# Performance work log

Hardware: AMD Instinct MI355X
Metric: run time of the kernel (lower is better)

## Reference

```python
import jax, jax.numpy as jnp
import numpy as np

EMBED_DIM = 1024
NUM_HEADS = 16
HEAD_DIM = EMBED_DIM // NUM_HEADS


def setup_inputs() -> dict:
    key = jax.random.key(0)
    ks = jax.random.split(key, 9)
    B, S, E, Hd = 1, 4096, EMBED_DIM, HEAD_DIM
    s = 0.02
    return {
        "x": jax.random.normal(ks[0], (B, S, E), jnp.float32),
        "mask": jnp.ones((B, S, S), jnp.int32),
        "Wq": jax.random.normal(ks[1], (E, E), jnp.float32) * s,
        "bq": jnp.zeros((E,), jnp.float32),
        "Wk": jax.random.normal(ks[2], (E, Hd), jnp.float32) * s,
        "bk": jnp.zeros((Hd,), jnp.float32),
        "Wv": jax.random.normal(ks[3], (E, Hd), jnp.float32) * s,
        "bv": jnp.zeros((Hd,), jnp.float32),
        "Wo": jax.random.normal(ks[4], (E, E), jnp.float32) * s,
        "bo": jnp.zeros((E,), jnp.float32),
    }


def reference(x, mask, Wq, bq, Wk, bk, Wv, bv, Wo, bo):
    B, S, E = x.shape
    H, Hd = NUM_HEADS, HEAD_DIM
    q = (x @ Wq + bq).reshape(B, S, H, Hd).transpose(0, 2, 1, 3)  # [B,H,S,Hd]
    k = x @ Wk + bk  # [B,S,Hd] single KV head (MQA)
    v = x @ Wv + bv  # [B,S,Hd]
    scale = 1.0 / np.sqrt(Hd).astype(np.float32)
    # broadcast single-head K across all query heads
    qk = jnp.einsum('bhqd,bkd->bhqk', q, k) * scale  # [B,H,S,S]
    qk = jnp.where(mask[:, None, :, :] == 0, jnp.float32(-10000.0), qk)
    attn = jax.nn.softmax(qk, axis=-1)
    out = jnp.einsum('bhqk,bkd->bhqd', attn, v)  # [B,H,S,Hd]
    out = out.transpose(0, 2, 1, 3).reshape(B, S, E)
    return out @ Wo + bo
```

## Files before the change

### kernel.cpp

```cpp
#include <hip/hip_runtime.h>
#include <hip/hip_bf16.h>
#include <stdint.h>

typedef __bf16 bf16x8 __attribute__((ext_vector_type(8)));
typedef float f32x4 __attribute__((ext_vector_type(4)));
typedef float f32x16 __attribute__((ext_vector_type(16)));
typedef unsigned int uint2v __attribute__((ext_vector_type(2)));

#define E_DIM 1024
#define HD 64
#define NH 16
#define QKV_LD 1152
#define LOG2E 1.44269504088896f

__device__ __forceinline__ float toF(float x) { return x; }
__device__ __forceinline__ float toF(__hip_bfloat16 x) { return __bfloat162float(x); }
__device__ __forceinline__ void storeOut(float* p, float v) { *p = v; }
__device__ __forceinline__ void storeOut(__hip_bfloat16* p, float v) { *p = __float2bfloat16(v); }

__device__ __forceinline__ unsigned cvtpk_bf16(float lo, float hi_) {
    unsigned r;
    asm("v_cvt_pk_bf16_f32 %0, %1, %2" : "=v"(r) : "v"(lo), "v"(hi_));
    return r;
}
__device__ __forceinline__ void perm32swap(unsigned& a, unsigned& b) {
    uint2v r = __builtin_amdgcn_permlane32_swap(a, b, false, false);
    a = r.x; b = r.y;
}
__device__ __forceinline__ float fexp2(float x) {
    float r;
    asm("v_exp_f32 %0, %1" : "=v"(r) : "v"(x));
    return r;
}

typedef __attribute__((address_space(1))) void gvoid;
typedef __attribute__((address_space(3))) void lvoid;
__device__ __forceinline__ void gload_lds16(const void* g, void* l) {
    __builtin_amdgcn_global_load_lds((gvoid*)g, (lvoid*)l, 16, 0, 0);
}

__global__ void cast_f32_bf16_kernel(const float* __restrict__ in, __hip_bfloat16* __restrict__ o, int n) {
    int i = (blockIdx.x * blockDim.x + threadIdx.x) * 4;
    if (i + 3 < n) {
        float4 v = *reinterpret_cast<const float4*>(in + i);
        __hip_bfloat16 t[4] = {__float2bfloat16(v.x), __float2bfloat16(v.y),
                               __float2bfloat16(v.z), __float2bfloat16(v.w)};
        *reinterpret_cast<uint2*>(o + i) = *reinterpret_cast<uint2*>(t);
    }
}

template<typename InT>
__global__ void transpose_cast_kernel(const InT* __restrict__ in, int ldi,
                                      __hip_bfloat16* __restrict__ out, int ldo,
                                      int R, int C) {
    __shared__ float tile[32][33];
    const int bx = blockIdx.x * 32;
    const int by = blockIdx.y * 32;
    const int tx = threadIdx.x & 31, ty = threadIdx.x >> 5;
#pragma unroll
    for (int j = 0; j < 4; ++j) {
        int r = bx + ty + j * 8, c = by + tx;
        tile[ty + j * 8][tx] = toF(in[(size_t)r * ldi + c]);
    }
    __syncthreads();
#pragma unroll
    for (int j = 0; j < 4; ++j) {
        int c = by + ty + j * 8, r = bx + tx;
        out[(size_t)c * ldo + r] = __float2bfloat16(tile[tx][ty + j * 8]);
    }
}

__global__ void concat_bias3_kernel(const float* __restrict__ bq, const float* __restrict__ bk,
                                    const float* __restrict__ bv, float* __restrict__ bqkv) {
    int i = blockIdx.x * blockDim.x + threadIdx.x;
    if (i < E_DIM) bqkv[i] = bq[i];
    else if (i < E_DIM + HD) bqkv[i] = bk[i - E_DIM];
    else if (i < E_DIM + 2 * HD) bqkv[i] = bv[i - E_DIM - HD];
}

__global__ void maskbits_kernel(const int* __restrict__ mask, unsigned long long* __restrict__ mb,
                                int nwords) {
    int gtid = blockIdx.x * blockDim.x + threadIdx.x;
    int wid = gtid >> 6, lane = gtid & 63;
    int nw = (gridDim.x * blockDim.x) >> 6;
    for (int w = wid; w < nwords; w += nw) {
        int v = mask[(size_t)w * 64 + lane];
        unsigned long long b = __ballot(v != 0);
        if (lane == 0) mb[w] = b;
    }
}

template<typename OutT>
__global__ __launch_bounds__(256)
void gemm_bt2_kernel(const __hip_bfloat16* __restrict__ A,
                     const __hip_bfloat16* __restrict__ Bt,
                     const float* __restrict__ bias,
                     OutT* __restrict__ C,
                     int M, int N, int K, float sQ, int nQ, float sKV) {
    constexpr int BM = 128, BN = 128, BK = 64;
    __shared__ __align__(16) unsigned char lA[2][BM * BK * 2];
    __shared__ __align__(16) unsigned char lB[2][BN * BK * 2];
    const int ntn = N / BN;
    const int tm = blockIdx.x / ntn, tn = blockIdx.x % ntn;
    const int tid = threadIdx.x, lane = tid & 63, wave = tid >> 6;
    const int l15 = lane & 15, l4 = lane >> 4;
    const int wm = (wave >> 1) * 64, wn = (wave & 1) * 64;
    const int r0 = tm * BM, c0 = tn * BN;
    const int NK = K / BK;

    size_t aoff[4], boff[4];
    unsigned ldso[4];
#pragma unroll
    for (int i = 0; i < 4; ++i) {
        int row = wave * 32 + i * 8 + (lane >> 3);
        int c = (lane & 7) ^ (row & 7);
        aoff[i] = (size_t)(r0 + row) * K * 2 + c * 16;
        boff[i] = (size_t)(c0 + row) * K * 2 + c * 16;
        ldso[i] = wave * 4096 + i * 1024;
    }
    const char* Ab = (const char*)A;
    const char* Bb = (const char*)Bt;

#pragma unroll
    for (int i = 0; i < 4; ++i) {
        gload_lds16(Ab + aoff[i], &lA[0][ldso[i]]);
        gload_lds16(Bb + boff[i], &lB[0][ldso[i]]);
    }
    __syncthreads();

    f32x4 z4 = {0.f, 0.f, 0.f, 0.f};
    f32x4 acc[4][4];
#pragma unroll
    for (int mi = 0; mi < 4; ++mi)
#pragma unroll
        for (int ni = 0; ni < 4; ++ni) acc[mi][ni] = z4;

    int buf = 0;
    for (int ks = 0; ks < NK; ++ks) {
        if (ks + 1 < NK) {
            size_t kb = (size_t)(ks + 1) * BK * 2;
#pragma unroll
            for (int i = 0; i < 4; ++i) {
                gload_lds16(Ab + aoff[i] + kb, &lA[buf ^ 1][ldso[i]]);
                gload_lds16(Bb + boff[i] + kb, &lB[buf ^ 1][ldso[i]]);
            }
        }
        bf16x8 af[4][2], bf[4][2];
#pragma unroll
        for (int mi = 0; mi < 4; ++mi) {
            int row = wm + mi * 16 + l15;
#pragma unroll
            for (int kh = 0; kh < 2; ++kh) {
                int slot = (kh * 4 + l4) ^ (row & 7);
                af[mi][kh] = *reinterpret_cast<const bf16x8*>(&lA[buf][row * 128 + slot * 16]);
            }
        }
#pragma unroll
        for (int ni = 0; ni < 4; ++ni) {
            int row = wn + ni * 16 + l15;
#pragma unroll
            for (int kh = 0; kh < 2; ++kh) {
                int slot = (kh * 4 + l4) ^ (row & 7);
                bf[ni][kh] = *reinterpret_cast<const bf16x8*>(&lB[buf][row * 128 + slot * 16]);
            }
        }
        __builtin_amdgcn_s_setprio(1);
#pragma unroll
        for (int mi = 0; mi < 4; ++mi)
#pragma unroll
            for (int ni = 0; ni < 4; ++ni) {
                acc[mi][ni] = __builtin_amdgcn_mfma_f32_16x16x32_bf16(af[mi][0], bf[ni][0], acc[mi][ni], 0, 0, 0);
                acc[mi][ni] = __builtin_amdgcn_mfma_f32_16x16x32_bf16(af[mi][1], bf[ni][1], acc[mi][ni], 0, 0, 0);
            }
        __builtin_amdgcn_s_setprio(0);
        __syncthreads();
        buf ^= 1;
    }

#pragma unroll
    for (int ni = 0; ni < 4; ++ni) {
        int col = c0 + wn + ni * 16 + l15;
        float b = bias[col];
        float s = (col < nQ) ? sQ : sKV;
#pragma unroll
        for (int mi = 0; mi < 4; ++mi) {
            int row = r0 + wm + mi * 16 + l4 * 4;
#pragma unroll
            for (int r = 0; r < 4; ++r) {
                float v = (acc[mi][ni][r] + b) * s;
                storeOut(C + (size_t)(row + r) * N + col, v);
            }
        }
    }
}

__global__ __launch_bounds__(256, 2)
void mqa5_kernel(const __hip_bfloat16* __restrict__ qkv,
                 const __hip_bfloat16* __restrict__ vtb,
                 const unsigned long long* __restrict__ mbits,
                 __hip_bfloat16* __restrict__ attnb,
                 int S) {
    __shared__ __align__(16) unsigned char sKV[2][32768];
    const int tid = threadIdx.x, lane = tid & 63, w = tid >> 6;
    const int r31 = lane & 31, hi = lane >> 5, rx = r31 & 15;
    const int q0 = blockIdx.x * 32;
    const int h = blockIdx.y * 4 + w;
    const int NT = S / 128, NW64 = S / 64;
    const __hip_bfloat16* kvb = qkv + E_DIM;

    bf16x8 qf[4];
    {
        const __hip_bfloat16* qp = qkv + (size_t)(q0 + r31) * QKV_LD + h * HD + hi * 8;
#pragma unroll
        for (int s = 0; s < 4; ++s) qf[s] = *reinterpret_cast<const bf16x8*>(qp + 16 * s);
    }

    const char* gbase[8];
    int gstep[8];
    unsigned ldsoff[8];
#pragma unroll
    for (int i = 0; i < 8; ++i) {
        int r = w * 32 + i * 4 + (lane >> 4);
        int sl = lane & 15;
        int c = sl ^ (r & 15);
        if (c < 8) {
            gbase[i] = (const char*)(kvb + (size_t)r * QKV_LD + c * 8);
            gstep[i] = 128 * QKV_LD * 2;
        } else {
            gbase[i] = (const char*)(vtb + (size_t)(r & 63) * S + (r >> 6) * 64 + (c - 8) * 8);
            gstep[i] = 128 * 2;
        }
        ldsoff[i] = w * 8192 + i * 1024;
    }

#pragma unroll
    for (int i = 0; i < 8; ++i) { gload_lds16(gbase[i], &sKV[0][ldsoff[i]]); gbase[i] += gstep[i]; }
    __syncthreads();

    float rm = -3e38f, rl = 0.f;
    f32x16 oacc[2];
#pragma unroll
    for (int i = 0; i < 16; ++i) { oacc[0][i] = 0.f; oacc[1][i] = 0.f; }

    int buf = 0;
    for (int t = 0; t < NT; ++t) {
        if (t + 1 < NT) {
#pragma unroll
            for (int i = 0; i < 8; ++i) { gload_lds16(gbase[i], &sKV[buf ^ 1][ldsoff[i]]); gbase[i] += gstep[i]; }
        }
        ulonglong2 wb = *reinterpret_cast<const ulonglong2*>(
            mbits + (size_t)(q0 + r31) * NW64 + 2 * t);
        const unsigned char* bp = sKV[buf];

        f32x16 sacc[4];
        __builtin_amdgcn_s_setprio(1);
#pragma unroll
        for (int kb = 0; kb < 4; ++kb) {
            const unsigned char* rowp = bp + (kb * 32 + r31) * 256;
            f32x16 a;
#pragma unroll
            for (int i = 0; i < 16; ++i) a[i] = 0.f;
#pragma unroll
            for (int s = 0; s < 4; ++s) {
                int slot = (2 * s + hi) ^ rx;
                bf16x8 kf = *reinterpret_cast<const bf16x8*>(rowp + slot * 16);
                a = __builtin_amdgcn_mfma_f32_32x32x16_bf16(kf, qf[s], a, 0, 0, 0);
            }
            sacc[kb] = a;
        }
        __builtin_amdgcn_s_setprio(0);

        if ((wb.x & wb.y) != ~0ull) {
#pragma unroll
            for (int kb = 0; kb < 4; ++kb) {
                unsigned long long wv = (kb < 2) ? wb.x : wb.y;
                int base = (kb & 1) * 32;
#pragma unroll
                for (int r = 0; r < 16; ++r) {
                    int kl = base + (r & 3) + 8 * (r >> 2) + 4 * hi;
                    if (!((wv >> kl) & 1)) sacc[kb][r] = -14427.0f;
                }
            }
        }

        float t0[8];
#pragma unroll
        for (int j = 0; j < 8; ++j) {
            float a01 = fmaxf(fmaxf(sacc[0][j], sacc[0][j + 8]), fmaxf(sacc[1][j], sacc[1][j + 8]));
            float a23 = fmaxf(fmaxf(sacc[2][j], sacc[2][j + 8]), fmaxf(sacc[3][j], sacc[3][j + 8]));
            t0[j] = fmaxf(a01, a23);
        }
        float u0 = fmaxf(t0[0], t0[4]), u1 = fmaxf(t0[1], t0[5]);
        float u2 = fmaxf(t0[2], t0[6]), u3 = fmaxf(t0[3], t0[7]);
        float pmax = fmaxf(fmaxf(u0, u1), fmaxf(u2, u3));
        pmax = fmaxf(pmax, __shfl_xor(pmax, 32));

        if (!__all(pmax - rm <= 8.0f)) {
            float rmn = fmaxf(rm, pmax);
            float al = fexp2(rm - rmn);
            rl *= al;
#pragma unroll
            for (int r = 0; r < 16; ++r) { oacc[0][r] *= al; oacc[1][r] *= al; }
            rm = rmn;
        }

        float s0 = 0.f, s1 = 0.f, s2 = 0.f, s3 = 0.f;
#pragma unroll
        for (int kb = 0; kb < 4; ++kb) {
#pragma unroll
            for (int r = 0; r < 16; r += 4) {
                sacc[kb][r + 0] = fexp2(sacc[kb][r + 0] - rm); s0 += sacc[kb][r + 0];
                sacc[kb][r + 1] = fexp2(sacc[kb][r + 1] - rm); s1 += sacc[kb][r + 1];
                sacc[kb][r + 2] = fexp2(sacc[kb][r + 2] - rm); s2 += sacc[kb][r + 2];
                sacc[kb][r + 3] = fexp2(sacc[kb][r + 3] - rm); s3 += sacc[kb][r + 3];
            }
        }
        float sum = (s0 + s1) + (s2 + s3);
        sum += __shfl_xor(sum, 32);
        rl += sum;

        bf16x8 pa[8];
#pragma unroll
        for (int kb = 0; kb < 4; ++kb) {
#pragma unroll
            for (int half = 0; half < 2; ++half) {
                int b0 = half * 8;
                unsigned A = cvtpk_bf16(sacc[kb][b0 + 0], sacc[kb][b0 + 1]);
                unsigned B = cvtpk_bf16(sacc[kb][b0 + 2], sacc[kb][b0 + 3]);
                unsigned C = cvtpk_bf16(sacc[kb][b0 + 4], sacc[kb][b0 + 5]);
                unsigned D = cvtpk_bf16(sacc[kb][b0 + 6], sacc[kb][b0 + 7]);
                perm32swap(A, C);
                perm32swap(B, D);
                union { unsigned u[4]; bf16x8 v; } pk;
                pk.u[0] = A; pk.u[1] = B; pk.u[2] = C; pk.u[3] = D;
                pa[kb * 2 + half] = pk.v;
            }
        }

        __builtin_amdgcn_s_setprio(1);
#pragma unroll
        for (int db = 0; db < 2; ++db) {
            f32x16 a = oacc[db];
#pragma unroll
            for (int j = 0; j < 2; ++j) {
                const unsigned char* rowp = bp + (j * 64 + db * 32 + r31) * 256;
#pragma unroll
                for (int s = 0; s < 4; ++s) {
                    int slot = (8 + 2 * s + hi) ^ rx;
                    bf16x8 vf = *reinterpret_cast<const bf16x8*>(rowp + slot * 16);
                    a = __builtin_amdgcn_mfma_f32_32x32x16_bf16(vf, pa[j * 4 + s], a, 0, 0, 0);
                }
            }
            oacc[db] = a;
        }
        __builtin_amdgcn_s_setprio(0);

        __syncthreads();
        buf ^= 1;
    }

    float inv = 1.0f / rl;
    __hip_bfloat16* op = attnb + (size_t)(q0 + r31) * E_DIM + h * HD;
#pragma unroll
    for (int db = 0; db < 2; ++db)
#pragma unroll
        for (int m = 0; m < 4; ++m) {
            uint2 pk;
            pk.x = cvtpk_bf16(oacc[db][4 * m + 0] * inv, oacc[db][4 * m + 1] * inv);
            pk.y = cvtpk_bf16(oacc[db][4 * m + 2] * inv, oacc[db][4 * m + 3] * inv);
            *reinterpret_cast<uint2*>(op + db * 32 + m * 8 + hi * 4) = pk;
        }
}

extern "C" void kernel_launch(void* const* d_in, const int* in_sizes, int n_in,
                              void* d_out, int out_size, void* d_ws, size_t ws_size,
                              hipStream_t stream) {
    (void)n_in; (void)out_size; (void)ws_size;
    const float* x  = (const float*)d_in[0];
    const int* mask = (const int*)d_in[1];
    const float* Wq = (const float*)d_in[2];
    const float* bq = (const float*)d_in[3];
    const float* Wk = (const float*)d_in[4];
    const float* bk = (const float*)d_in[5];
    const float* Wv = (const float*)d_in[6];
    const float* bv = (const float*)d_in[7];
    const float* Wo = (const float*)d_in[8];
    const float* bo = (const float*)d_in[9];
    float* out = (float*)d_out;

    const int E = E_DIM;
    const int S = in_sizes[0] / E;

    char* ws = (char*)d_ws;
    size_t off = 0;
    auto alloc = [&](size_t b) { char* p = ws + off; off += (b + 255) & ~(size_t)255; return p; };
    __hip_bfloat16* xb     = (__hip_bfloat16*)alloc((size_t)S * E * 2);
    __hip_bfloat16* wqkvT  = (__hip_bfloat16*)alloc((size_t)QKV_LD * E * 2);
    __hip_bfloat16* woT    = (__hip_bfloat16*)alloc((size_t)E * E * 2);
    __hip_bfloat16* qkvb   = (__hip_bfloat16*)alloc((size_t)S * QKV_LD * 2);
    __hip_bfloat16* vtb    = (__hip_bfloat16*)alloc((size_t)HD * S * 2);
    __hip_bfloat16* attnb  = (__hip_bfloat16*)alloc((size_t)S * E * 2);
    float* bqkv  = (float*)alloc(QKV_LD * 4);
    unsigned long long* mbits = (unsigned long long*)alloc((size_t)S * (S / 64) * 8);

    cast_f32_bf16_kernel<<<dim3((S * E / 4 + 255) / 256), dim3(256), 0, stream>>>(x, xb, S * E);
    transpose_cast_kernel<float><<<dim3(E / 32, E / 32), dim3(256), 0, stream>>>(Wq, E, wqkvT, E, E, E);
    transpose_cast_kernel<float><<<dim3(E / 32, HD / 32), dim3(256), 0, stream>>>(
        Wk, HD, wqkvT + (size_t)E * E, E, E, HD);
    transpose_cast_kernel<float><<<dim3(E / 32, HD / 32), dim3(256), 0, stream>>>(
        Wv, HD, wqkvT + (size_t)(E + HD) * E, E, E, HD);
    transpose_cast_kernel<float><<<dim3(E / 32, E / 32), dim3(256), 0, stream>>>(Wo, E, woT, E, E, E);
    concat_bias3_kernel<<<dim3((QKV_LD + 255) / 256), dim3(256), 0, stream>>>(bq, bk, bv, bqkv);
    maskbits_kernel<<<dim3(1024), dim3(256), 0, stream>>>(mask, mbits, S * (S / 64));

    gemm_bt2_kernel<__hip_bfloat16><<<dim3((S / 128) * (QKV_LD / 128)), dim3(256), 0, stream>>>(
        xb, wqkvT, bqkv, qkvb, S, QKV_LD, E, 0.125f * LOG2E, E, 1.0f);
    transpose_cast_kernel<__hip_bfloat16><<<dim3(S / 32, HD / 32), dim3(256), 0, stream>>>(
        qkvb + E + HD, QKV_LD, vtb, S, S, HD);
    mqa5_kernel<<<dim3(S / 32, NH / 4), dim3(256), 0, stream>>>(qkvb, vtb, mbits, attnb, S);
    gemm_bt2_kernel<float><<<dim3((S / 128) * (E / 128)), dim3(256), 0, stream>>>(
        attnb, woT, bo, out, S, E, E, 1.0f, E, 1.0f);
}
```

Baseline: 181.1 us.

## Compute softmax row sums with MFMA, merge weight transposes, restructure PV loop

```diff
diff --git a/kernel.cpp b/kernel.cpp
--- a/kernel.cpp
+++ b/kernel.cpp
@@ -67,6 +67,35 @@
     for (int j = 0; j < 4; ++j) {
         int c = by + ty + j * 8, r = bx + tx;
         out[(size_t)c * ldo + r] = __float2bfloat16(tile[tx][ty + j * 8]);
+    }
+}
+
+__global__ __launch_bounds__(256)
+void transpose4_kernel(const float* __restrict__ Wq, const float* __restrict__ Wk,
+                       const float* __restrict__ Wv, const float* __restrict__ Wo,
+                       __hip_bfloat16* __restrict__ wqkvT, __hip_bfloat16* __restrict__ woT) {
+    const int z = blockIdx.z;
+    const float* in; __hip_bfloat16* out; int ldi;
+    if (z == 0)      { in = Wq; out = wqkvT;                                ldi = E_DIM; }
+    else if (z == 1) { if (blockIdx.y >= HD / 32) return;
+                       in = Wk; out = wqkvT + (size_t)E_DIM * E_DIM;        ldi = HD; }
+    else if (z == 2) { if (blockIdx.y >= HD / 32) return;
+                       in = Wv; out = wqkvT + (size_t)(E_DIM + HD) * E_DIM; ldi = HD; }
+    else             { in = Wo; out = woT;                                  ldi = E_DIM; }
+    __shared__ float tile[32][33];
+    const int bx = blockIdx.x * 32;
+    const int by = blockIdx.y * 32;
+    const int tx = threadIdx.x & 31, ty = threadIdx.x >> 5;
+#pragma unroll
+    for (int j = 0; j < 4; ++j) {
+        int r = bx + ty + j * 8, c = by + tx;
+        tile[ty + j * 8][tx] = in[(size_t)r * ldi + c];
+    }
+    __syncthreads();
+#pragma unroll
+    for (int j = 0; j < 4; ++j) {
+        int c = by + ty + j * 8, r = bx + tx;
+        out[(size_t)c * E_DIM + r] = __float2bfloat16(tile[tx][ty + j * 8]);
     }
 }
 
@@ -194,8 +223,8 @@
     }
 }
 
-__global__ __launch_bounds__(256, 2)
-void mqa5_kernel(const __hip_bfloat16* __restrict__ qkv,
+__global__ __launch_bounds__(256) __attribute__((amdgpu_waves_per_eu(2, 2)))
+void mqa7_kernel(const __hip_bfloat16* __restrict__ qkv,
                  const __hip_bfloat16* __restrict__ vtb,
                  const unsigned long long* __restrict__ mbits,
                  __hip_bfloat16* __restrict__ attnb,
@@ -214,6 +243,9 @@
 #pragma unroll
         for (int s = 0; s < 4; ++s) qf[s] = *reinterpret_cast<const bf16x8*>(qp + 16 * s);
     }
+    bf16x8 ones;
+#pragma unroll
+    for (int i = 0; i < 8; ++i) ones[i] = (__bf16)1.0f;
 
     const char* gbase[8];
     int gstep[8];
@@ -237,19 +269,19 @@
     for (int i = 0; i < 8; ++i) { gload_lds16(gbase[i], &sKV[0][ldsoff[i]]); gbase[i] += gstep[i]; }
     __syncthreads();
 
-    float rm = -3e38f, rl = 0.f;
-    f32x16 oacc[2];
-#pragma unroll
-    for (int i = 0; i < 16; ++i) { oacc[0][i] = 0.f; oacc[1][i] = 0.f; }
-
+    float rm = -3e38f;
+    f32x16 oacc[2], lacc;
+#pragma unroll
+    for (int i = 0; i < 16; ++i) { oacc[0][i] = 0.f; oacc[1][i] = 0.f; lacc[i] = 0.f; }
+
+    const size_t mrow = (size_t)(q0 + r31) * NW64;
     int buf = 0;
     for (int t = 0; t < NT; ++t) {
+        ulonglong2 wb = *reinterpret_cast<const ulonglong2*>(mbits + mrow + 2 * t);
         if (t + 1 < NT) {
 #pragma unroll
             for (int i = 0; i < 8; ++i) { gload_lds16(gbase[i], &sKV[buf ^ 1][ldsoff[i]]); gbase[i] += gstep[i]; }
         }
-        ulonglong2 wb = *reinterpret_cast<const ulonglong2*>(
-            mbits + (size_t)(q0 + r31) * NW64 + 2 * t);
         const unsigned char* bp = sKV[buf];
 
         f32x16 sacc[4];
@@ -286,80 +318,73 @@
         float t0[8];
 #pragma unroll
         for (int j = 0; j < 8; ++j) {
-            float a01 = fmaxf(fmaxf(sacc[0][j], sacc[0][j + 8]), fmaxf(sacc[1][j], sacc[1][j + 8]));
-            float a23 = fmaxf(fmaxf(sacc[2][j], sacc[2][j + 8]), fmaxf(sacc[3][j], sacc[3][j + 8]));
-            t0[j] = fmaxf(a01, a23);
-        }
-        float u0 = fmaxf(t0[0], t0[4]), u1 = fmaxf(t0[1], t0[5]);
-        float u2 = fmaxf(t0[2], t0[6]), u3 = fmaxf(t0[3], t0[7]);
-        float pmax = fmaxf(fmaxf(u0, u1), fmaxf(u2, u3));
-        pmax = fmaxf(pmax, __shfl_xor(pmax, 32));
+            float a = fmaxf(fmaxf(sacc[0][j], sacc[0][j + 8]), sacc[1][j]);
+            float b = fmaxf(fmaxf(sacc[1][j + 8], sacc[2][j]), sacc[2][j + 8]);
+            float c = fmaxf(fmaxf(sacc[3][j], sacc[3][j + 8]), a);
+            t0[j] = fmaxf(b, c);
+        }
+        float u0 = fmaxf(fmaxf(t0[0], t0[1]), t0[2]);
+        float u1 = fmaxf(fmaxf(t0[3], t0[4]), t0[5]);
+        float pmax = fmaxf(fmaxf(t0[6], t0[7]), fmaxf(u0, u1));
 
         if (!__all(pmax - rm <= 8.0f)) {
-            float rmn = fmaxf(rm, pmax);
+            float pm2 = fmaxf(pmax, __shfl_xor(pmax, 32));
+            float rmn = fmaxf(rm, pm2);
             float al = fexp2(rm - rmn);
-            rl *= al;
-#pragma unroll
-            for (int r = 0; r < 16; ++r) { oacc[0][r] *= al; oacc[1][r] *= al; }
+#pragma unroll
+            for (int r = 0; r < 16; ++r) { oacc[0][r] *= al; oacc[1][r] *= al; lacc[r] *= al; }
             rm = rmn;
         }
 
-        float s0 = 0.f, s1 = 0.f, s2 = 0.f, s3 = 0.f;
-#pragma unroll
-        for (int kb = 0; kb < 4; ++kb) {
-#pragma unroll
-            for (int r = 0; r < 16; r += 4) {
-                sacc[kb][r + 0] = fexp2(sacc[kb][r + 0] - rm); s0 += sacc[kb][r + 0];
-                sacc[kb][r + 1] = fexp2(sacc[kb][r + 1] - rm); s1 += sacc[kb][r + 1];
-                sacc[kb][r + 2] = fexp2(sacc[kb][r + 2] - rm); s2 += sacc[kb][r + 2];
-                sacc[kb][r + 3] = fexp2(sacc[kb][r + 3] - rm); s3 += sacc[kb][r + 3];
-            }
-        }
-        float sum = (s0 + s1) + (s2 + s3);
-        sum += __shfl_xor(sum, 32);
-        rl += sum;
-
-        bf16x8 pa[8];
-#pragma unroll
-        for (int kb = 0; kb < 4; ++kb) {
-#pragma unroll
-            for (int half = 0; half < 2; ++half) {
-                int b0 = half * 8;
-                unsigned A = cvtpk_bf16(sacc[kb][b0 + 0], sacc[kb][b0 + 1]);
-                unsigned B = cvtpk_bf16(sacc[kb][b0 + 2], sacc[kb][b0 + 3]);
-                unsigned C = cvtpk_bf16(sacc[kb][b0 + 4], sacc[kb][b0 + 5]);
-                unsigned D = cvtpk_bf16(sacc[kb][b0 + 6], sacc[kb][b0 + 7]);
-                perm32swap(A, C);
-                perm32swap(B, D);
-                union { unsigned u[4]; bf16x8 v; } pk;
-                pk.u[0] = A; pk.u[1] = B; pk.u[2] = C; pk.u[3] = D;
-                pa[kb * 2 + half] = pk.v;
-            }
-        }
-
-        __builtin_amdgcn_s_setprio(1);
-#pragma unroll
-        for (int db = 0; db < 2; ++db) {
-            f32x16 a = oacc[db];
-#pragma unroll
-            for (int j = 0; j < 2; ++j) {
+#pragma unroll
+        for (int kb = 0; kb < 4; ++kb)
+#pragma unroll
+            for (int r = 0; r < 16; ++r) sacc[kb][r] = fexp2(sacc[kb][r] - rm);
+
+#pragma unroll
+        for (int j = 0; j < 2; ++j) {
+            bf16x8 pa[4];
+#pragma unroll
+            for (int kk = 0; kk < 2; ++kk) {
+#pragma unroll
+                for (int half = 0; half < 2; ++half) {
+                    int b0 = half * 8;
+                    const f32x16& sv = sacc[2 * j + kk];
+                    unsigned A = cvtpk_bf16(sv[b0 + 0], sv[b0 + 1]);
+                    unsigned B = cvtpk_bf16(sv[b0 + 2], sv[b0 + 3]);
+                    unsigned C = cvtpk_bf16(sv[b0 + 4], sv[b0 + 5]);
+                    unsigned D = cvtpk_bf16(sv[b0 + 6], sv[b0 + 7]);
+                    perm32swap(A, C);
+                    perm32swap(B, D);
+                    union { unsigned u[4]; bf16x8 v; } pk;
+                    pk.u[0] = A; pk.u[1] = B; pk.u[2] = C; pk.u[3] = D;
+                    pa[kk * 2 + half] = pk.v;
+                }
+            }
+            __builtin_amdgcn_s_setprio(1);
+#pragma unroll
+            for (int db = 0; db < 2; ++db) {
                 const unsigned char* rowp = bp + (j * 64 + db * 32 + r31) * 256;
+                f32x16 a = oacc[db];
 #pragma unroll
                 for (int s = 0; s < 4; ++s) {
                     int slot = (8 + 2 * s + hi) ^ rx;
                     bf16x8 vf = *reinterpret_cast<const bf16x8*>(rowp + slot * 16);
-                    a = __builtin_amdgcn_mfma_f32_32x32x16_bf16(vf, pa[j * 4 + s], a, 0, 0, 0);
+                    a = __builtin_amdgcn_mfma_f32_32x32x16_bf16(vf, pa[s], a, 0, 0, 0);
                 }
-            }
-            oacc[db] = a;
-        }
-        __builtin_amdgcn_s_setprio(0);
+                oacc[db] = a;
+            }
+#pragma unroll
+            for (int s = 0; s < 4; ++s)
+                lacc = __builtin_amdgcn_mfma_f32_32x32x16_bf16(ones, pa[s], lacc, 0, 0, 0);
+            __builtin_amdgcn_s_setprio(0);
+        }
 
         __syncthreads();
         buf ^= 1;
     }
 
-    float inv = 1.0f / rl;
+    float inv = 1.0f / lacc[0];
     __hip_bfloat16* op = attnb + (size_t)(q0 + r31) * E_DIM + h * HD;
 #pragma unroll
     for (int db = 0; db < 2; ++db)
@@ -404,12 +429,7 @@
     unsigned long long* mbits = (unsigned long long*)alloc((size_t)S * (S / 64) * 8);
 
     cast_f32_bf16_kernel<<<dim3((S * E / 4 + 255) / 256), dim3(256), 0, stream>>>(x, xb, S * E);
-    transpose_cast_kernel<float><<<dim3(E / 32, E / 32), dim3(256), 0, stream>>>(Wq, E, wqkvT, E, E, E);
-    transpose_cast_kernel<float><<<dim3(E / 32, HD / 32), dim3(256), 0, stream>>>(
-        Wk, HD, wqkvT + (size_t)E * E, E, E, HD);
-    transpose_cast_kernel<float><<<dim3(E / 32, HD / 32), dim3(256), 0, stream>>>(
-        Wv, HD, wqkvT + (size_t)(E + HD) * E, E, E, HD);
-    transpose_cast_kernel<float><<<dim3(E / 32, E / 32), dim3(256), 0, stream>>>(Wo, E, woT, E, E, E);
+    transpose4_kernel<<<dim3(E / 32, E / 32, 4), dim3(256), 0, stream>>>(Wq, Wk, Wv, Wo, wqkvT, woT);
     concat_bias3_kernel<<<dim3((QKV_LD + 255) / 256), dim3(256), 0, stream>>>(bq, bk, bv, bqkv);
     maskbits_kernel<<<dim3(1024), dim3(256), 0, stream>>>(mask, mbits, S * (S / 64));
 
@@ -417,7 +437,7 @@
         xb, wqkvT, bqkv, qkvb, S, QKV_LD, E, 0.125f * LOG2E, E, 1.0f);
     transpose_cast_kernel<__hip_bfloat16><<<dim3(S / 32, HD / 32), dim3(256), 0, stream>>>(
         qkvb + E + HD, QKV_LD, vtb, S, S, HD);
-    mqa5_kernel<<<dim3(S / 32, NH / 4), dim3(256), 0, stream>>>(qkvb, vtb, mbits, attnb, S);
+    mqa7_kernel<<<dim3(S / 32, NH / 4), dim3(256), 0, stream>>>(qkvb, vtb, mbits, attnb, S);
     gemm_bt2_kernel<float><<<dim3((S / 128) * (E / 128)), dim3(256), 0, stream>>>(
         attnb, woT, bo, out, S, E, E, 1.0f, E, 1.0f);
 }
```

After: 176.5 us. 2.5% less time.
